# Kernel tuning notes

Measured on AMD Instinct MI355X. Metric: run time of the kernel, lower is better.

The kernel has to match this reference:

```python
import math
import jax, jax.numpy as jnp
import numpy as np

D, H, L, DFF, V = 512, 8, 6, 2048, 32000
B, S = 2, 2048
PAD = 1


def _layernorm(x, g, b, eps=1e-5):
    m = x.mean(-1, keepdims=True)
    v = ((x - m) ** 2).mean(-1, keepdims=True)
    return (x - m) / jnp.sqrt(v + eps) * g + b


def _mha(qx, kx, w, b, mask, h=H):
    # w: [4, D, D] (q,k,v,out), b: [4, D]; mask broadcastable to [B,1,Sq,Sk]
    bs, sq, d = qx.shape
    dk = d // h
    def proj(x, i):
        return (x @ w[i] + b[i]).reshape(bs, -1, h, dk).transpose(0, 2, 1, 3)
    q, k, v = proj(qx, 0), proj(kx, 1), proj(kx, 2)
    scores = jnp.einsum('bhqd,bhkd->bhqk', q, k) / math.sqrt(dk)
    scores = jnp.where(mask, scores, -jnp.inf)
    attn = jax.nn.softmax(scores, axis=-1)
    out = jnp.einsum('bhqk,bhkd->bhqd', attn, v).transpose(0, 2, 1, 3).reshape(bs, sq, d)
    return out @ w[3] + b[3]


def _ff(x, w1, b1, w2, b2):
    return jax.nn.relu(x @ w1 + b1) @ w2 + b2


def _sinusoidal_pe(max_len, d):
    pos = np.arange(max_len)[:, None].astype(np.float64)
    div = np.exp(np.arange(0, d, 2) * (-math.log(10000.0) / d))
    pe = np.zeros((max_len, d), np.float32)
    pe[:, 0::2] = np.sin(pos * div)
    pe[:, 1::2] = np.cos(pos * div)
    return jnp.asarray(pe[None])  # [1, max_len, d]


def setup_inputs() -> dict:
    key = jax.random.key(0)
    ks = iter(jax.random.split(key, 32))
    def w(shape):
        return jax.random.normal(next(ks), shape, jnp.float32) * 0.02
    inp = {
        'src': jax.random.randint(next(ks), (B, S), 2, V),
        'tgt': jax.random.randint(next(ks), (B, S), 2, V),
        'src_emb': w((V, D)),
        'tgt_emb': w((V, D)),
        'pe': _sinusoidal_pe(S, D),
        'enc_attn_w': w((L, 4, D, D)), 'enc_attn_b': jnp.zeros((L, 4, D)),
        'enc_ff_w1': w((L, D, DFF)), 'enc_ff_b1': jnp.zeros((L, DFF)),
        'enc_ff_w2': w((L, DFF, D)), 'enc_ff_b2': jnp.zeros((L, D)),
        'enc_ln_g': jnp.ones((L, 2, D)), 'enc_ln_b': jnp.zeros((L, 2, D)),
        'dec_self_w': w((L, 4, D, D)), 'dec_self_b': jnp.zeros((L, 4, D)),
        'dec_src_w': w((L, 4, D, D)), 'dec_src_b': jnp.zeros((L, 4, D)),
        'dec_ff_w1': w((L, D, DFF)), 'dec_ff_b1': jnp.zeros((L, DFF)),
        'dec_ff_w2': w((L, DFF, D)), 'dec_ff_b2': jnp.zeros((L, D)),
        'dec_ln_g': jnp.ones((L, 3, D)), 'dec_ln_b': jnp.zeros((L, 3, D)),
        'ln_g': jnp.ones((D,)), 'ln_b': jnp.zeros((D,)),
        'fc_w': w((D, V)), 'fc_b': jnp.zeros((V,)),
    }
    return inp


def reference(src, tgt, src_emb, tgt_emb, pe,
              enc_attn_w, enc_attn_b, enc_ff_w1, enc_ff_b1, enc_ff_w2, enc_ff_b2,
              enc_ln_g, enc_ln_b,
              dec_self_w, dec_self_b, dec_src_w, dec_src_b,
              dec_ff_w1, dec_ff_b1, dec_ff_w2, dec_ff_b2, dec_ln_g, dec_ln_b,
              ln_g, ln_b, fc_w, fc_b):
    s_len, t_len = src.shape[1], tgt.shape[1]
    src_mask = (src != PAD)[:, None, None, :]                      # [B,1,1,Ss]
    tril = jnp.tril(jnp.ones((t_len, t_len), bool))
    tgt_mask = (tgt != PAD)[:, None, None, :] & tril[None, None]   # [B,1,St,St]

    x = src_emb[src] + pe[:, :s_len]
    for l in range(L):
        x2 = _layernorm(x, enc_ln_g[l, 0], enc_ln_b[l, 0])
        x = x + _mha(x2, x2, enc_attn_w[l], enc_attn_b[l], src_mask)
        x2 = _layernorm(x, enc_ln_g[l, 1], enc_ln_b[l, 1])
        x = x + _ff(x2, enc_ff_w1[l], enc_ff_b1[l], enc_ff_w2[l], enc_ff_b2[l])
    memory = x

    y = tgt_emb[tgt] + pe[:, :t_len]
    for l in range(L):
        y2 = _layernorm(y, dec_ln_g[l, 0], dec_ln_b[l, 0])
        y = y + _mha(y2, y2, dec_self_w[l], dec_self_b[l], tgt_mask)
        y2 = _layernorm(y, dec_ln_g[l, 1], dec_ln_b[l, 1])
        y = y + _mha(y2, memory, dec_src_w[l], dec_src_b[l], src_mask)
        y2 = _layernorm(y, dec_ln_g[l, 2], dec_ln_b[l, 2])
        y = y + _ff(y2, dec_ff_w1[l], dec_ff_b1[l], dec_ff_w2[l], dec_ff_b2[l])

    return _layernorm(y, ln_g, ln_b) @ fc_w + fc_b  # [B, St, V]
```

## Files before the change

### kernel.cpp

```cpp
#include <hip/hip_runtime.h>
#include <math.h>

#define D_MODEL 512
#define NHEAD   8
#define NLAYER  6
#define DFF_    2048
#define VOCAB   32000
#define BATCH   2
#define SEQ     2048
#define NTOK    (BATCH*SEQ)
#define PAD_ID  1

typedef __attribute__((ext_vector_type(8))) short s16x8;
typedef __attribute__((ext_vector_type(4))) float f32x4;
typedef unsigned short u16;
typedef unsigned int   u32;
typedef unsigned long long u64;

__device__ __forceinline__ u16 f2bf(float x) {
  u32 u = __builtin_bit_cast(u32, x);
  u += 0x7FFFu + ((u >> 16) & 1u);
  return (u16)(u >> 16);
}

__device__ __forceinline__ float exp2i(float x) {
  float r; asm("v_exp_f32 %0, %1" : "=v"(r) : "v"(x)); return r;
}

__device__ __forceinline__ void gload16(const void* g, void* l) {
  __builtin_amdgcn_global_load_lds(
      (const __attribute__((address_space(1))) u32*)g,
      (__attribute__((address_space(3))) u32*)l, 16, 0, 0);
}

#define CEXP 0.1803368802f

__global__ __launch_bounds__(256) void embed2_kernel(
    const int* __restrict__ src, const int* __restrict__ tgt,
    const float* __restrict__ se, const float* __restrict__ te,
    const float* __restrict__ pe, float* __restrict__ xe, float* __restrict__ yd)
{
  const int z = blockIdx.y;
  const int* tok = z ? tgt : src;
  const float* emb = z ? te : se;
  float* out = z ? yd : xe;
  const int total = NTOK * D_MODEL;
  for (int i = blockIdx.x * 256 + threadIdx.x; i < total; i += gridDim.x * 256) {
    int t = i >> 9;
    int d = i & 511;
    int s = t & (SEQ - 1);
    out[i] = emb[(size_t)tok[t] * D_MODEL + d] + pe[(size_t)s * D_MODEL + d];
  }
}

__global__ __launch_bounds__(64) void padmask2_kernel(
    const int* __restrict__ src, const int* __restrict__ tgt,
    u64* __restrict__ pmS, u64* __restrict__ pmT)
{
  const int z = blockIdx.z;
  const int* tok = z ? tgt : src;
  u64* pm = z ? pmT : pmS;
  int b = blockIdx.y, t = blockIdx.x;
  int lane = threadIdx.x;
  u64 m = __ballot(tok[(size_t)b * SEQ + t * 64 + lane] != PAD_ID);
  if (lane == 0) pm[b * (SEQ / 64) + t] = m;
}

__global__ __launch_bounds__(256) void ln_kernel(
    const float* __restrict__ x, const float* __restrict__ g,
    const float* __restrict__ bb, u16* __restrict__ y)
{
  __shared__ float red[8];
  const size_t row = blockIdx.x;
  const float* xr = x + row * D_MODEL;
  u16* yr = y + row * D_MODEL;
  const int t = threadIdx.x;
  float a0 = xr[t], a1 = xr[t + 256];
  float s = a0 + a1;
  #pragma unroll
  for (int o = 32; o > 0; o >>= 1) s += __shfl_down(s, o, 64);
  int wv = t >> 6, ln = t & 63;
  if (ln == 0) red[wv] = s;
  __syncthreads();
  if (t == 0) red[4] = red[0] + red[1] + red[2] + red[3];
  __syncthreads();
  float mean = red[4] * (1.0f / D_MODEL);
  float d0 = a0 - mean, d1 = a1 - mean;
  float vs = d0 * d0 + d1 * d1;
  #pragma unroll
  for (int o = 32; o > 0; o >>= 1) vs += __shfl_down(vs, o, 64);
  if (ln == 0) red[wv] = vs;
  __syncthreads();
  if (t == 0) red[5] = red[0] + red[1] + red[2] + red[3];
  __syncthreads();
  float inv = rsqrtf(red[5] * (1.0f / D_MODEL) + 1e-5f);
  yr[t]       = f2bf(d0 * inv * g[t]       + bb[t]);
  yr[t + 256] = f2bf(d1 * inv * g[t + 256] + bb[t + 256]);
}

__global__ __launch_bounds__(256) void tconv2_kernel(
    const float* __restrict__ s0, const float* __restrict__ s1,
    u16* __restrict__ d0, u16* __restrict__ d1, int zsplit, int K, int N)
{
  __shared__ float tile[64][65];
  const int z = blockIdx.z;
  const float* src = (z < zsplit) ? s0 + (size_t)z * K * N : s1 + (size_t)(z - zsplit) * K * N;
  u16* dst = (z < zsplit) ? d0 + (size_t)z * K * N : d1 + (size_t)(z - zsplit) * K * N;
  const int n0 = blockIdx.x * 64, k0 = blockIdx.y * 64;
  const int t = threadIdx.x;
  const int cr = t >> 4, cc = (t & 15) * 4;
  #pragma unroll
  for (int it = 0; it < 4; ++it) {
    int kr = cr + it * 16;
    float4 v = *(const float4*)&src[(size_t)(k0 + kr) * N + n0 + cc];
    tile[kr][cc] = v.x; tile[kr][cc + 1] = v.y; tile[kr][cc + 2] = v.z; tile[kr][cc + 3] = v.w;
  }
  __syncthreads();
  #pragma unroll
  for (int it = 0; it < 4; ++it) {
    int nr = cr + it * 16;
    u32 lo = (u32)f2bf(tile[cc + 0][nr]) | ((u32)f2bf(tile[cc + 1][nr]) << 16);
    u32 hi = (u32)f2bf(tile[cc + 2][nr]) | ((u32)f2bf(tile[cc + 3][nr]) << 16);
    uint2 pk; pk.x = lo; pk.y = hi;
    *(uint2*)&dst[(size_t)(n0 + nr) * K + k0 + cc] = pk;
  }
}

__global__ __launch_bounds__(256) void tconv3_kernel(
    const float* __restrict__ s0, const float* __restrict__ s1,
    const float* __restrict__ s2, u16* __restrict__ dst0)
{
  __shared__ float tile[64][65];
  const int z = blockIdx.z;
  const float* src = (z < 24) ? s0 + (size_t)z * 262144
                   : (z < 48) ? s1 + (size_t)(z - 24) * 262144
                              : s2 + (size_t)(z - 48) * 262144;
  u16* dst = dst0 + (size_t)z * 262144;
  const int n0 = blockIdx.x * 64, k0 = blockIdx.y * 64;
  const int t = threadIdx.x;
  const int cr = t >> 4, cc = (t & 15) * 4;
  #pragma unroll
  for (int it = 0; it < 4; ++it) {
    int kr = cr + it * 16;
    float4 v = *(const float4*)&src[(size_t)(k0 + kr) * 512 + n0 + cc];
    tile[kr][cc] = v.x; tile[kr][cc + 1] = v.y; tile[kr][cc + 2] = v.z; tile[kr][cc + 3] = v.w;
  }
  __syncthreads();
  #pragma unroll
  for (int it = 0; it < 4; ++it) {
    int nr = cr + it * 16;
    u32 lo = (u32)f2bf(tile[cc + 0][nr]) | ((u32)f2bf(tile[cc + 1][nr]) << 16);
    u32 hi = (u32)f2bf(tile[cc + 2][nr]) | ((u32)f2bf(tile[cc + 3][nr]) << 16);
    uint2 pk; pk.x = lo; pk.y = hi;
    *(uint2*)&dst[(size_t)(n0 + nr) * 512 + k0 + cc] = pk;
  }
}

template<int MODE, int BM, int BN, int MAP>
__global__ __launch_bounds__(256, 2) void mm_kernel(
    const u16* __restrict__ A, const u16* __restrict__ Wt,
    const float* __restrict__ bias, const float* __restrict__ res,
    void* __restrict__ Cout, u16* __restrict__ vtOut,
    int M, int N, int K,
    long long wStride, long long bStride, long long cStride)
{
  constexpr int MI = BM / 32;
  constexpr int NI = BN / 32;
  constexpr bool DB = (BM == 64 && BN == 64);
  __shared__ u16 sh[(DB ? 2 : 1) * (BM + BN) * 64];
  const int z = blockIdx.z;
  size_t wOff, bOff;
  if (MAP == 1) {
    wOff = (size_t)(z >> 1) * 4 * 262144 + (size_t)(1 + (z & 1)) * 262144;
    bOff = (size_t)(z >> 1) * 4 * 512 + (size_t)(1 + (z & 1)) * 512;
  } else {
    wOff = (size_t)z * wStride;
    bOff = (size_t)z * bStride;
  }
  Wt += wOff;
  bias += bOff;
  const int bm = blockIdx.y * BM, bn = blockIdx.x * BN;
  const int tid = threadIdx.x, lane = tid & 63, w = tid >> 6;
  const int wm = w >> 1, wn = w & 1;
  const int l15 = lane & 15, l4 = lane >> 4;
  const int wrow0 = wm * (BM / 2), wcol0 = wn * (BN / 2);
  const u16* aBase = A  + (size_t)bm * K;
  const u16* bBase = Wt + (size_t)bn * K;
  f32x4 acc[MI][NI] = {};

  auto mfma_step = [&](const u16* Asb, const u16* Bsb) {
    #pragma unroll
    for (int ks = 0; ks < 2; ++ks) {
      s16x8 af[MI], bf[NI];
      #pragma unroll
      for (int mi = 0; mi < MI; ++mi) {
        int rr = wrow0 + mi * 16 + l15;
        af[mi] = *(const s16x8*)&Asb[(rr << 6) + (((ks * 4 + l4) ^ (rr & 7)) << 3)];
      }
      #pragma unroll
      for (int ni = 0; ni < NI; ++ni) {
        int rr = wcol0 + ni * 16 + l15;
        bf[ni] = *(const s16x8*)&Bsb[(rr << 6) + (((ks * 4 + l4) ^ (rr & 7)) << 3)];
      }
      #pragma unroll
      for (int mi = 0; mi < MI; ++mi)
        #pragma unroll
        for (int ni = 0; ni < NI; ++ni)
          acc[mi][ni] = __builtin_amdgcn_mfma_f32_16x16x32_bf16(af[mi], bf[ni], acc[mi][ni], 0, 0, 0);
    }
  };

  if constexpr (DB) {
    u16* As0 = sh;
    u16* As1 = sh + 64 * 64;
    u16* Bs0 = sh + 2 * 64 * 64;
    u16* Bs1 = sh + 3 * 64 * 64;
    auto stage = [&](int k0, u16* Ad, u16* Bd) {
      #pragma unroll
      for (int i = 0; i < 2; ++i) {
        int lin = i * 256 + tid;
        int r = lin >> 3, sp = lin & 7;
        gload16(aBase + (size_t)r * K + k0 + ((sp ^ (r & 7)) * 8), &Ad[(i * 256 + w * 64) * 8]);
      }
      #pragma unroll
      for (int i = 0; i < 2; ++i) {
        int lin = i * 256 + tid;
        int r = lin >> 3, sp = lin & 7;
        gload16(bBase + (size_t)r * K + k0 + ((sp ^ (r & 7)) * 8), &Bd[(i * 256 + w * 64) * 8]);
      }
    };
    stage(0, As0, Bs0);
    __syncthreads();
    const int nt = K >> 6;
    for (int t = 0; t < nt; ++t) {
      const bool even = !(t & 1);
      u16* Ac = even ? As0 : As1;
      u16* Bc = even ? Bs0 : Bs1;
      if (t + 1 < nt) stage((t + 1) << 6, even ? As1 : As0, even ? Bs1 : Bs0);
      mfma_step(Ac, Bc);
      __syncthreads();
    }
  } else {
    u16* As = sh;
    u16* Bs = sh + BM * 64;
    for (int k0 = 0; k0 < K; k0 += 64) {
      #pragma unroll
      for (int i = 0; i < BM / 32; ++i) {
        int lin = i * 256 + tid;
        int r = lin >> 3, sp = lin & 7;
        gload16(aBase + (size_t)r * K + k0 + ((sp ^ (r & 7)) * 8), &As[(i * 256 + w * 64) * 8]);
      }
      #pragma unroll
      for (int i = 0; i < BN / 32; ++i) {
        int lin = i * 256 + tid;
        int r = lin >> 3, sp = lin & 7;
        gload16(bBase + (size_t)r * K + k0 + ((sp ^ (r & 7)) * 8), &Bs[(i * 256 + w * 64) * 8]);
      }
      __syncthreads();
      mfma_step(As, Bs);
      __syncthreads();
    }
  }

  const bool vpath = (MODE == 4 && z == 2) || (MODE == 5 && (z & 1) == 1);
  if (vpath) {
    u16* TT = sh;
    #pragma unroll
    for (int mi = 0; mi < MI; ++mi)
      #pragma unroll
      for (int ni = 0; ni < NI; ++ni)
        #pragma unroll
        for (int r = 0; r < 4; ++r) {
          int rowl = wrow0 + mi * 16 + l4 * 4 + r;
          int coll = wcol0 + ni * 16 + l15;
          TT[coll * 72 + rowl] = f2bf(acc[mi][ni][r] + bias[bn + coll]);
        }
    __syncthreads();
    const int b = bm >> 11, s0loc = bm & 2047, h = bn >> 6;
    const int layer = (MODE == 5) ? (z >> 1) : 0;
    u16* vbase = vtOut + (size_t)layer * ((size_t)NTOK * D_MODEL)
               + ((size_t)(b * NHEAD + h) * 64) * SEQ;
    int d = tid >> 2, sc = (tid & 3) * 16;
    s16x8 v0 = *(const s16x8*)&TT[d * 72 + sc];
    s16x8 v1 = *(const s16x8*)&TT[d * 72 + sc + 8];
    *(s16x8*)(vbase + (size_t)d * SEQ + s0loc + sc) = v0;
    *(s16x8*)(vbase + (size_t)d * SEQ + s0loc + sc + 8) = v1;
    return;
  }

  const int zi = (MAP == 1) ? (z >> 1) : z;
  #pragma unroll
  for (int ni = 0; ni < NI; ++ni) {
    int col = bn + wcol0 + ni * 16 + l15;
    float bb = bias[col];
    #pragma unroll
    for (int mi = 0; mi < MI; ++mi) {
      #pragma unroll
      for (int r = 0; r < 4; ++r) {
        int row = bm + wrow0 + mi * 16 + l4 * 4 + r;
        size_t off = (size_t)zi * cStride + (size_t)row * N + col;
        float v = acc[mi][ni][r] + bb;
        if (MODE == 1 || MODE == 6) v += res[(size_t)row * N + col];
        if (MODE == 3) v = fmaxf(v, 0.0f);
        if (MODE <= 1 || MODE == 6) ((float*)Cout)[off] = v;
        else                        ((u16*)Cout)[off] = f2bf(v);
        if (MODE == 6) vtOut[(size_t)row * N + col] = f2bf(v);
      }
    }
  }
}

template<int CAUSAL, int QPROJ>
__global__ __launch_bounds__(256, 2) void fattn_kernel(
    const u16* __restrict__ Qg, const u16* __restrict__ Kg,
    const u16* __restrict__ Vt, const u16* __restrict__ Wq,
    const float* __restrict__ qbias, const u64* __restrict__ padm,
    u16* __restrict__ Og)
{
  __shared__ u16 Ks[2][128 * 64];
  __shared__ u16 Vs[2][64 * 128];
  __shared__ u16 Ps[4][16 * 128];
  const int qtile = CAUSAL ? (int)(gridDim.x - 1 - blockIdx.x) : (int)blockIdx.x;
  const int qt = qtile * 64;
  const int h = blockIdx.y, b = blockIdx.z;
  const int tid = threadIdx.x, lane = tid & 63, w = tid >> 6;
  const int l15 = lane & 15, l4 = lane >> 4;
  const int hoff = h * 64;
  const u16* Kbase = Kg + (size_t)(b * SEQ) * D_MODEL + hoff;
  const u16* Vbase = Vt + (size_t)(b * NHEAD + h) * 64 * SEQ;
  const u64* pmb = padm + b * (SEQ / 64);

  s16x8 aq[2];
  if constexpr (QPROJ) {
    const u16* xBase = Qg + (size_t)(b * SEQ + qt) * D_MODEL;
    const u16* wBase = Wq + (size_t)hoff * D_MODEL;
    u16* Xs = Ks[0];
    u16* Wsh = Ks[0] + 64 * 64;
    f32x4 qa[4] = {};
    for (int k0 = 0; k0 < 512; k0 += 64) {
      #pragma unroll
      for (int i = 0; i < 2; ++i) {
        int lin = i * 256 + tid;
        int r = lin >> 3, sp = lin & 7;
        gload16(xBase + (size_t)r * D_MODEL + k0 + ((sp ^ (r & 7)) * 8), &Xs[(i * 256 + w * 64) * 8]);
      }
      #pragma unroll
      for (int i = 0; i < 2; ++i) {
        int lin = i * 256 + tid;
        int r = lin >> 3, sp = lin & 7;
        gload16(wBase + (size_t)r * D_MODEL + k0 + ((sp ^ (r & 7)) * 8), &Wsh[(i * 256 + w * 64) * 8]);
      }
      __syncthreads();
      #pragma unroll
      for (int ks = 0; ks < 2; ++ks) {
        int rr = w * 16 + l15;
        s16x8 xa = *(const s16x8*)&Xs[(rr << 6) + (((ks * 4 + l4) ^ (rr & 7)) << 3)];
        #pragma unroll
        for (int ni = 0; ni < 4; ++ni) {
          int rw = ni * 16 + l15;
          s16x8 wb = *(const s16x8*)&Wsh[(rw << 6) + (((ks * 4 + l4) ^ (rw & 7)) << 3)];
          qa[ni] = __builtin_amdgcn_mfma_f32_16x16x32_bf16(xa, wb, qa[ni], 0, 0, 0);
        }
      }
      __syncthreads();
    }
    u16* Qsh = (u16*)Ps;
    #pragma unroll
    for (int ni = 0; ni < 4; ++ni) {
      int col = ni * 16 + l15;
      float bb = qbias[hoff + col];
      #pragma unroll
      for (int r = 0; r < 4; ++r) {
        int row = w * 16 + l4 * 4 + r;
        Qsh[(row << 6) + ((((col >> 3)) ^ (row & 7)) << 3) + (col & 7)] = f2bf(qa[ni][r] + bb);
      }
    }
    __syncthreads();
    {
      int rr = w * 16 + l15;
      aq[0] = *(const s16x8*)&Qsh[(rr << 6) + (((0 + l4) ^ (rr & 7)) << 3)];
      aq[1] = *(const s16x8*)&Qsh[(rr << 6) + (((4 + l4) ^ (rr & 7)) << 3)];
    }
  } else {
    const u16* qp = Qg + (size_t)(b * SEQ + qt + w * 16 + l15) * D_MODEL + hoff + l4 * 8;
    aq[0] = *(const s16x8*)qp;
    aq[1] = *(const s16x8*)(qp + 32);
  }

  f32x4 oacc[4] = {};
  float mrow[4] = {-1e30f, -1e30f, -1e30f, -1e30f};
  float lrow[4] = {0.f, 0.f, 0.f, 0.f};
  const int nt = CAUSAL ? (qt >> 7) + 1 : SEQ / 128;

  #define STAGE(KV0, BUF)                                                              \
    {                                                                                  \
      _Pragma("unroll")                                                                \
      for (int it = 0; it < 4; ++it) {                                                 \
        int lin = it * 256 + tid;                                                      \
        int rr = lin >> 3, sp = lin & 7;                                               \
        gload16(Kbase + (size_t)((KV0) + rr) * D_MODEL + ((sp ^ (rr & 7)) * 8),        \
                &Ks[BUF][(it * 256 + w * 64) * 8]);                                    \
      }                                                                                \
      _Pragma("unroll")                                                                \
      for (int it = 0; it < 4; ++it) {                                                 \
        int lin = it * 256 + tid;                                                      \
        int rr = lin >> 4, ko = lin & 15;                                              \
        gload16(Vbase + (size_t)rr * SEQ + (KV0) + ((ko ^ (rr & 15)) * 8),             \
                &Vs[BUF][(it * 256 + w * 64) * 8]);                                    \
      }                                                                                \
    }

  if constexpr (QPROJ) __syncthreads();
  STAGE(0, 0);
  __syncthreads();

  for (int kt = 0; kt < nt; ++kt) {
    const int kv0 = kt * 128;
    const int cur = kt & 1;
    if (kt + 1 < nt) STAGE(kv0 + 128, cur ^ 1);

    f32x4 sac[8] = {};
    #pragma unroll
    for (int ks = 0; ks < 2; ++ks)
      #pragma unroll
      for (int jn = 0; jn < 8; ++jn) {
        int rr = jn * 16 + l15;
        s16x8 bk = *(const s16x8*)&Ks[cur][(rr << 6) + (((ks * 4 + l4) ^ (rr & 7)) << 3)];
        sac[jn] = __builtin_amdgcn_mfma_f32_16x16x32_bf16(aq[ks], bk, sac[jn], 0, 0, 0);
      }

    const u64 m0 = pmb[(kv0 >> 6)];
    const u64 m1 = pmb[(kv0 >> 6) + 1];
    const bool lastC = CAUSAL && (kt == nt - 1);
    if (((m0 & m1) != ~0ull) || lastC) {
      #pragma unroll
      for (int jn = 0; jn < 8; ++jn) {
        int kvg = kv0 + jn * 16 + l15;
        u64 mm = (jn < 4) ? m0 : m1;
        bool okp = (mm >> ((jn & 3) * 16 + l15)) & 1;
        #pragma unroll
        for (int r = 0; r < 4; ++r) {
          int qg = qt + w * 16 + l4 * 4 + r;
          bool ok = okp && (!CAUSAL || kvg <= qg);
          if (!ok) sac[jn][r] = -1e30f;
        }
      }
    }

    float mx[4];
    #pragma unroll
    for (int r = 0; r < 4; ++r) {
      float m = fmaxf(fmaxf(fmaxf(sac[0][r], sac[1][r]), fmaxf(sac[2][r], sac[3][r])),
                      fmaxf(fmaxf(sac[4][r], sac[5][r]), fmaxf(sac[6][r], sac[7][r])));
      #pragma unroll
      for (int o = 1; o < 16; o <<= 1) m = fmaxf(m, __shfl_xor(m, o, 16));
      mx[r] = m;
    }
    float growth = fmaxf(fmaxf(mx[0] - mrow[0], mx[1] - mrow[1]),
                         fmaxf(mx[2] - mrow[2], mx[3] - mrow[3]));
    if (__any(growth > 64.0f)) {
      #pragma unroll
      for (int r = 0; r < 4; ++r) {
        float mn = fmaxf(mrow[r], mx[r]);
        float sc = exp2i((mrow[r] - mn) * CEXP);
        mrow[r] = mn;
        lrow[r] *= sc;
        #pragma unroll
        for (int jn = 0; jn < 4; ++jn) oacc[jn][r] *= sc;
      }
    }

    #pragma unroll
    for (int r = 0; r < 4; ++r) {
      const int prow = l4 * 4 + r;
      float rs = 0.f;
      #pragma unroll
      for (int jn = 0; jn < 8; ++jn) {
        float pv = exp2i((sac[jn][r] - mrow[r]) * CEXP);
        rs += pv;
        int g = ((jn * 2 + (l15 >> 3)) ^ prow) & 15;
        Ps[w][prow * 128 + g * 8 + (l15 & 7)] = f2bf(pv);
      }
      #pragma unroll
      for (int o = 1; o < 16; o <<= 1) rs += __shfl_xor(rs, o, 16);
      lrow[r] += rs;
    }

    #pragma unroll
    for (int kslot = 0; kslot < 4; ++kslot) {
      s16x8 pa = *(const s16x8*)&Ps[w][l15 * 128 + ((((kslot * 4 + l4) ^ l15) & 15) << 3)];
      #pragma unroll
      for (int jn = 0; jn < 4; ++jn) {
        int rr = jn * 16 + l15;
        s16x8 bv = *(const s16x8*)&Vs[cur][(rr << 7) + (((kslot * 4 + l4) ^ (rr & 15)) << 3)];
        oacc[jn] = __builtin_amdgcn_mfma_f32_16x16x32_bf16(pa, bv, oacc[jn], 0, 0, 0);
      }
    }
    __syncthreads();
  }
  #undef STAGE

  float inv[4];
  #pragma unroll
  for (int r = 0; r < 4; ++r) inv[r] = 1.0f / lrow[r];
  #pragma unroll
  for (int jn = 0; jn < 4; ++jn)
    #pragma unroll
    for (int r = 0; r < 4; ++r)
      Og[(size_t)(b * SEQ + qt + w * 16 + l4 * 4 + r) * D_MODEL + hoff + jn * 16 + l15] =
          f2bf(oacc[jn][r] * inv[r]);
}

extern "C" void kernel_launch(void* const* d_in, const int* in_sizes, int n_in,
                              void* d_out, int out_size, void* d_ws, size_t ws_size,
                              hipStream_t stream)
{
  const int*   src        = (const int*)  d_in[0];
  const int*   tgt        = (const int*)  d_in[1];
  const float* src_emb    = (const float*)d_in[2];
  const float* tgt_emb    = (const float*)d_in[3];
  const float* pe         = (const float*)d_in[4];
  const float* enc_attn_w = (const float*)d_in[5];
  const float* enc_attn_b = (const float*)d_in[6];
  const float* enc_ff_w1  = (const float*)d_in[7];
  const float* enc_ff_b1  = (const float*)d_in[8];
  const float* enc_ff_w2  = (const float*)d_in[9];
  const float* enc_ff_b2  = (const float*)d_in[10];
  const float* enc_ln_g   = (const float*)d_in[11];
  const float* enc_ln_bb  = (const float*)d_in[12];
  const float* dec_self_w = (const float*)d_in[13];
  const float* dec_self_b = (const float*)d_in[14];
  const float* dec_src_w  = (const float*)d_in[15];
  const float* dec_src_b  = (const float*)d_in[16];
  const float* dec_ff_w1  = (const float*)d_in[17];
  const float* dec_ff_b1  = (const float*)d_in[18];
  const float* dec_ff_w2  = (const float*)d_in[19];
  const float* dec_ff_b2  = (const float*)d_in[20];
  const float* dec_ln_g   = (const float*)d_in[21];
  const float* dec_ln_bb  = (const float*)d_in[22];
  const float* fin_ln_g   = (const float*)d_in[23];
  const float* fin_ln_b   = (const float*)d_in[24];
  const float* fc_w       = (const float*)d_in[25];
  const float* fc_b       = (const float*)d_in[26];
  float* out = (float*)d_out;

  const size_t DD = (size_t)D_MODEL * D_MODEL;
  const size_t FD = (size_t)D_MODEL * DFF_;
  const size_t TD = (size_t)NTOK * D_MODEL;

  char* ob = (char*)d_out;
  size_t off = 0;
  auto alloco = [&](size_t bytes) { void* p = ob + off; off += (bytes + 255) & ~(size_t)255; return p; };
  u16* wt_enc_attn = (u16*)alloco(24 * DD * 2);
  u16* wt_dec_self = (u16*)alloco(24 * DD * 2);
  u16* wt_dec_src  = (u16*)alloco(24 * DD * 2);
  u16* wt_enc_ff1  = (u16*)alloco(6 * FD * 2);
  u16* wt_enc_ff2  = (u16*)alloco(6 * FD * 2);
  u16* wt_dec_ff1  = (u16*)alloco(6 * FD * 2);
  u16* wt_dec_ff2  = (u16*)alloco(6 * FD * 2);
  u16* qb   = (u16*)alloco(2 * TD * 2);
  u16* kb   = qb + TD;
  u16* vtb  = (u16*)alloco(TD * 2);
  u16* aob  = (u16*)alloco(TD * 2);
  u16* hbb  = (u16*)alloco((size_t)NTOK * DFF_ * 2);
  u16* memb = (u16*)alloco(TD * 2);
  u16* ckb  = (u16*)alloco(6 * TD * 2);
  u16* cvtb = (u16*)alloco(6 * TD * 2);

  char* wsb = (char*)d_ws;
  u16*   fcwt = (u16*)wsb;
  size_t wo = ((size_t)VOCAB * D_MODEL * 2 + 255) & ~(size_t)255;
  float* xe  = (float*)(wsb + wo); wo += TD * 4;
  float* yd  = (float*)(wsb + wo); wo += TD * 4;
  u16*   x2b = (u16*)(wsb + wo);   wo += TD * 2;
  u64*   pmS = (u64*)(wsb + wo);   wo += 1024;
  u64*   pmT = (u64*)(wsb + wo);

  dim3 blk(256);
  dim3 gN512(8, 64, 1), gQKV(8, 64, 3), gCKV(8, 64, 12);
  dim3 gFF1(16, 32, 1), gFC(125, 32, 1);
  dim3 gAttn(SEQ / 64, NHEAD, BATCH);
  const long long llDD = (long long)DD, llTD = (long long)TD;

  padmask2_kernel<<<dim3(SEQ / 64, BATCH, 2), dim3(64), 0, stream>>>(src, tgt, pmS, pmT);
  tconv3_kernel<<<dim3(8, 8, 72), blk, 0, stream>>>(enc_attn_w, dec_self_w, dec_src_w, wt_enc_attn);
  tconv2_kernel<<<dim3(32, 8, 12), blk, 0, stream>>>(enc_ff_w1, dec_ff_w1, wt_enc_ff1, wt_dec_ff1, 6, 512, 2048);
  tconv2_kernel<<<dim3(8, 32, 12), blk, 0, stream>>>(enc_ff_w2, dec_ff_w2, wt_enc_ff2, wt_dec_ff2, 6, 2048, 512);
  tconv2_kernel<<<dim3(500, 8, 1), blk, 0, stream>>>(fc_w, fc_w, fcwt, fcwt, 1, 512, VOCAB);
  embed2_kernel<<<dim3(2048, 2), blk, 0, stream>>>(src, tgt, src_emb, tgt_emb, pe, xe, yd);

  for (int l = 0; l < NLAYER; ++l) {
    ln_kernel<<<dim3(NTOK), blk, 0, stream>>>(xe, enc_ln_g + (size_t)(l * 2 + 0) * D_MODEL,
                                              enc_ln_bb + (size_t)(l * 2 + 0) * D_MODEL, x2b);
    mm_kernel<4, 64, 64, 0><<<gQKV, blk, 0, stream>>>(x2b, wt_enc_attn + (size_t)l * 4 * DD,
        enc_attn_b + (size_t)l * 4 * D_MODEL, nullptr, qb, vtb, NTOK, 512, 512, llDD, D_MODEL, llTD);
    fattn_kernel<0, 0><<<gAttn, blk, 0, stream>>>(qb, kb, vtb, nullptr, nullptr, pmS, aob);
    mm_kernel<1, 64, 64, 0><<<gN512, blk, 0, stream>>>(aob, wt_enc_attn + (size_t)(l * 4 + 3) * DD,
        enc_attn_b + (size_t)(l * 4 + 3) * D_MODEL, xe, xe, nullptr, NTOK, 512, 512, 0, 0, 0);
    ln_kernel<<<dim3(NTOK), blk, 0, stream>>>(xe, enc_ln_g + (size_t)(l * 2 + 1) * D_MODEL,
                                              enc_ln_bb + (size_t)(l * 2 + 1) * D_MODEL, x2b);
    mm_kernel<3, 128, 128, 0><<<gFF1, blk, 0, stream>>>(x2b, wt_enc_ff1 + (size_t)l * FD,
        enc_ff_b1 + (size_t)l * DFF_, nullptr, hbb, nullptr, NTOK, DFF_, 512, 0, 0, 0);
    if (l == NLAYER - 1)
      mm_kernel<6, 64, 64, 0><<<gN512, blk, 0, stream>>>(hbb, wt_enc_ff2 + (size_t)l * FD,
          enc_ff_b2 + (size_t)l * D_MODEL, xe, xe, memb, NTOK, 512, DFF_, 0, 0, 0);
    else
      mm_kernel<1, 64, 64, 0><<<gN512, blk, 0, stream>>>(hbb, wt_enc_ff2 + (size_t)l * FD,
          enc_ff_b2 + (size_t)l * D_MODEL, xe, xe, nullptr, NTOK, 512, DFF_, 0, 0, 0);
  }

  mm_kernel<5, 64, 64, 1><<<gCKV, blk, 0, stream>>>(memb, wt_dec_src, dec_src_b, nullptr,
      ckb, cvtb, NTOK, 512, 512, 0, 0, llTD);

  for (int l = 0; l < NLAYER; ++l) {
    const u16* Ws = wt_dec_self + (size_t)l * 4 * DD;
    const u16* Wc = wt_dec_src + (size_t)l * 4 * DD;
    const float* bs  = dec_self_b + (size_t)l * 4 * D_MODEL;
    const float* bcb = dec_src_b + (size_t)l * 4 * D_MODEL;
    ln_kernel<<<dim3(NTOK), blk, 0, stream>>>(yd, dec_ln_g + (size_t)(l * 3 + 0) * D_MODEL,
                                              dec_ln_bb + (size_t)(l * 3 + 0) * D_MODEL, x2b);
    mm_kernel<4, 64, 64, 0><<<gQKV, blk, 0, stream>>>(x2b, Ws, bs, nullptr, qb, vtb,
                                                      NTOK, 512, 512, llDD, D_MODEL, llTD);
    fattn_kernel<1, 0><<<gAttn, blk, 0, stream>>>(qb, kb, vtb, nullptr, nullptr, pmT, aob);
    mm_kernel<1, 64, 64, 0><<<gN512, blk, 0, stream>>>(aob, Ws + 3 * DD, bs + 3 * D_MODEL, yd, yd,
                                                       nullptr, NTOK, 512, 512, 0, 0, 0);
    ln_kernel<<<dim3(NTOK), blk, 0, stream>>>(yd, dec_ln_g + (size_t)(l * 3 + 1) * D_MODEL,
                                              dec_ln_bb + (size_t)(l * 3 + 1) * D_MODEL, x2b);
    fattn_kernel<0, 1><<<gAttn, blk, 0, stream>>>(x2b, ckb + (size_t)l * TD, cvtb + (size_t)l * TD,
                                                  Wc, bcb, pmS, aob);
    mm_kernel<1, 64, 64, 0><<<gN512, blk, 0, stream>>>(aob, Wc + 3 * DD, bcb + 3 * D_MODEL, yd, yd,
                                                       nullptr, NTOK, 512, 512, 0, 0, 0);
    ln_kernel<<<dim3(NTOK), blk, 0, stream>>>(yd, dec_ln_g + (size_t)(l * 3 + 2) * D_MODEL,
                                              dec_ln_bb + (size_t)(l * 3 + 2) * D_MODEL, x2b);
    mm_kernel<3, 128, 128, 0><<<gFF1, blk, 0, stream>>>(x2b, wt_dec_ff1 + (size_t)l * FD,
        dec_ff_b1 + (size_t)l * DFF_, nullptr, hbb, nullptr, NTOK, DFF_, 512, 0, 0, 0);
    mm_kernel<1, 64, 64, 0><<<gN512, blk, 0, stream>>>(hbb, wt_dec_ff2 + (size_t)l * FD,
        dec_ff_b2 + (size_t)l * D_MODEL, yd, yd, nullptr, NTOK, 512, DFF_, 0, 0, 0);
  }

  ln_kernel<<<dim3(NTOK), blk, 0, stream>>>(yd, fin_ln_g, fin_ln_b, x2b);
  mm_kernel<0, 128, 256, 0><<<gFC, blk, 0, stream>>>(x2b, fcwt, fc_b, nullptr, out, nullptr,
                                                     NTOK, VOCAB, 512, 0, 0, 0);

  (void)in_sizes; (void)n_in; (void)out_size; (void)ws_size;
}
```

Measured before the change: 2.503 ms.

## Transpose attention MFMA operands and make LayerNorm one row per wavefront

The flash-attention kernel swaps the MFMA operand order so each lane holds scores for a single query row. That collapses the per-row max and sum to scalar state with two cross-lane shuffles, and lets P and output stores use packed vector writes. LayerNorm now processes four rows per block, one wavefront each, with vectorized float4 loads and single-pass sum and sum-of-squares reductions, removing shared memory and barriers. The single-pass variance formula is slightly less numerically robust than the two-pass version.

```diff
diff --git a/kernel.cpp b/kernel.cpp
--- a/kernel.cpp
+++ b/kernel.cpp
@@ -70,32 +70,31 @@
     const float* __restrict__ x, const float* __restrict__ g,
     const float* __restrict__ bb, u16* __restrict__ y)
 {
-  __shared__ float red[8];
-  const size_t row = blockIdx.x;
-  const float* xr = x + row * D_MODEL;
-  u16* yr = y + row * D_MODEL;
-  const int t = threadIdx.x;
-  float a0 = xr[t], a1 = xr[t + 256];
-  float s = a0 + a1;
+  const int lane = threadIdx.x & 63;
+  const size_t row = (size_t)blockIdx.x * 4 + (threadIdx.x >> 6);
+  const float* xr = x + row * D_MODEL + lane * 8;
+  float4 v0 = *(const float4*)xr;
+  float4 v1 = *(const float4*)(xr + 4);
+  float sum = (v0.x + v0.y) + (v0.z + v0.w) + (v1.x + v1.y) + (v1.z + v1.w);
+  float ss = v0.x * v0.x + v0.y * v0.y + v0.z * v0.z + v0.w * v0.w
+           + v1.x * v1.x + v1.y * v1.y + v1.z * v1.z + v1.w * v1.w;
   #pragma unroll
-  for (int o = 32; o > 0; o >>= 1) s += __shfl_down(s, o, 64);
-  int wv = t >> 6, ln = t & 63;
-  if (ln == 0) red[wv] = s;
-  __syncthreads();
-  if (t == 0) red[4] = red[0] + red[1] + red[2] + red[3];
-  __syncthreads();
-  float mean = red[4] * (1.0f / D_MODEL);
-  float d0 = a0 - mean, d1 = a1 - mean;
-  float vs = d0 * d0 + d1 * d1;
-  #pragma unroll
-  for (int o = 32; o > 0; o >>= 1) vs += __shfl_down(vs, o, 64);
-  if (ln == 0) red[wv] = vs;
-  __syncthreads();
-  if (t == 0) red[5] = red[0] + red[1] + red[2] + red[3];
-  __syncthreads();
-  float inv = rsqrtf(red[5] * (1.0f / D_MODEL) + 1e-5f);
-  yr[t]       = f2bf(d0 * inv * g[t]       + bb[t]);
-  yr[t + 256] = f2bf(d1 * inv * g[t + 256] + bb[t + 256]);
+  for (int o = 1; o < 64; o <<= 1) {
+    sum += __shfl_xor(sum, o, 64);
+    ss  += __shfl_xor(ss, o, 64);
+  }
+  float mean = sum * (1.0f / D_MODEL);
+  float inv = rsqrtf(ss * (1.0f / D_MODEL) - mean * mean + 1e-5f);
+  float4 g0 = *(const float4*)&g[lane * 8];
+  float4 g1 = *(const float4*)&g[lane * 8 + 4];
+  float4 c0 = *(const float4*)&bb[lane * 8];
+  float4 c1 = *(const float4*)&bb[lane * 8 + 4];
+  uint4 o;
+  o.x = (u32)f2bf((v0.x - mean) * inv * g0.x + c0.x) | ((u32)f2bf((v0.y - mean) * inv * g0.y + c0.y) << 16);
+  o.y = (u32)f2bf((v0.z - mean) * inv * g0.z + c0.z) | ((u32)f2bf((v0.w - mean) * inv * g0.w + c0.w) << 16);
+  o.z = (u32)f2bf((v1.x - mean) * inv * g1.x + c1.x) | ((u32)f2bf((v1.y - mean) * inv * g1.y + c1.y) << 16);
+  o.w = (u32)f2bf((v1.z - mean) * inv * g1.z + c1.z) | ((u32)f2bf((v1.w - mean) * inv * g1.w + c1.w) << 16);
+  *(uint4*)&y[row * D_MODEL + lane * 8] = o;
 }
 
 __global__ __launch_bounds__(256) void tconv2_kernel(
@@ -329,6 +328,7 @@
   const u16* Kbase = Kg + (size_t)(b * SEQ) * D_MODEL + hoff;
   const u16* Vbase = Vt + (size_t)(b * NHEAD + h) * 64 * SEQ;
   const u64* pmb = padm + b * (SEQ / 64);
+  const int qg = qt + w * 16 + l15;
 
   s16x8 aq[2];
   if constexpr (QPROJ) {
@@ -382,14 +382,13 @@
       aq[1] = *(const s16x8*)&Qsh[(rr << 6) + (((4 + l4) ^ (rr & 7)) << 3)];
     }
   } else {
-    const u16* qp = Qg + (size_t)(b * SEQ + qt + w * 16 + l15) * D_MODEL + hoff + l4 * 8;
+    const u16* qp = Qg + (size_t)(b * SEQ + qg) * D_MODEL + hoff + l4 * 8;
     aq[0] = *(const s16x8*)qp;
     aq[1] = *(const s16x8*)(qp + 32);
   }
 
   f32x4 oacc[4] = {};
-  float mrow[4] = {-1e30f, -1e30f, -1e30f, -1e30f};
-  float lrow[4] = {0.f, 0.f, 0.f, 0.f};
+  float mrow = -1e30f, lrow = 0.f;
   const int nt = CAUSAL ? (qt >> 7) + 1 : SEQ / 128;
 
   #define STAGE(KV0, BUF)                                                              \
@@ -425,8 +424,8 @@
       #pragma unroll
       for (int jn = 0; jn < 8; ++jn) {
         int rr = jn * 16 + l15;
-        s16x8 bk = *(const s16x8*)&Ks[cur][(rr << 6) + (((ks * 4 + l4) ^ (rr & 7)) << 3)];
-        sac[jn] = __builtin_amdgcn_mfma_f32_16x16x32_bf16(aq[ks], bk, sac[jn], 0, 0, 0);
+        s16x8 ak = *(const s16x8*)&Ks[cur][(rr << 6) + (((ks * 4 + l4) ^ (rr & 7)) << 3)];
+        sac[jn] = __builtin_amdgcn_mfma_f32_16x16x32_bf16(ak, aq[ks], sac[jn], 0, 0, 0);
       }
 
     const u64 m0 = pmb[(kv0 >> 6)];
@@ -435,80 +434,78 @@
     if (((m0 & m1) != ~0ull) || lastC) {
       #pragma unroll
       for (int jn = 0; jn < 8; ++jn) {
-        int kvg = kv0 + jn * 16 + l15;
         u64 mm = (jn < 4) ? m0 : m1;
-        bool okp = (mm >> ((jn & 3) * 16 + l15)) & 1;
         #pragma unroll
         for (int r = 0; r < 4; ++r) {
-          int qg = qt + w * 16 + l4 * 4 + r;
-          bool ok = okp && (!CAUSAL || kvg <= qg);
+          int kl = (jn & 3) * 16 + l4 * 4 + r;
+          int kvg = kv0 + jn * 16 + l4 * 4 + r;
+          bool ok = ((mm >> kl) & 1) && (!CAUSAL || kvg <= qg);
           if (!ok) sac[jn][r] = -1e30f;
         }
       }
     }
 
-    float mx[4];
-    #pragma unroll
-    for (int r = 0; r < 4; ++r) {
-      float m = fmaxf(fmaxf(fmaxf(sac[0][r], sac[1][r]), fmaxf(sac[2][r], sac[3][r])),
-                      fmaxf(fmaxf(sac[4][r], sac[5][r]), fmaxf(sac[6][r], sac[7][r])));
-      #pragma unroll
-      for (int o = 1; o < 16; o <<= 1) m = fmaxf(m, __shfl_xor(m, o, 16));
-      mx[r] = m;
-    }
-    float growth = fmaxf(fmaxf(mx[0] - mrow[0], mx[1] - mrow[1]),
-                         fmaxf(mx[2] - mrow[2], mx[3] - mrow[3]));
-    if (__any(growth > 64.0f)) {
-      #pragma unroll
-      for (int r = 0; r < 4; ++r) {
-        float mn = fmaxf(mrow[r], mx[r]);
-        float sc = exp2i((mrow[r] - mn) * CEXP);
-        mrow[r] = mn;
-        lrow[r] *= sc;
+    float m = sac[0][0];
+    #pragma unroll
+    for (int jn = 0; jn < 8; ++jn)
+      #pragma unroll
+      for (int r = 0; r < 4; ++r) m = fmaxf(m, sac[jn][r]);
+    m = fmaxf(m, __shfl_xor(m, 16, 64));
+    m = fmaxf(m, __shfl_xor(m, 32, 64));
+
+    if (__any(m - mrow > 64.0f)) {
+      float mn = fmaxf(mrow, m);
+      float sc = exp2i((mrow - mn) * CEXP);
+      mrow = mn;
+      lrow *= sc;
+      #pragma unroll
+      for (int jn = 0; jn < 4; ++jn)
         #pragma unroll
-        for (int jn = 0; jn < 4; ++jn) oacc[jn][r] *= sc;
-      }
-    }
-
-    #pragma unroll
-    for (int r = 0; r < 4; ++r) {
-      const int prow = l4 * 4 + r;
-      float rs = 0.f;
-      #pragma unroll
-      for (int jn = 0; jn < 8; ++jn) {
-        float pv = exp2i((sac[jn][r] - mrow[r]) * CEXP);
-        rs += pv;
-        int g = ((jn * 2 + (l15 >> 3)) ^ prow) & 15;
-        Ps[w][prow * 128 + g * 8 + (l15 & 7)] = f2bf(pv);
-      }
-      #pragma unroll
-      for (int o = 1; o < 16; o <<= 1) rs += __shfl_xor(rs, o, 16);
-      lrow[r] += rs;
-    }
-
-    #pragma unroll
-    for (int kslot = 0; kslot < 4; ++kslot) {
-      s16x8 pa = *(const s16x8*)&Ps[w][l15 * 128 + ((((kslot * 4 + l4) ^ l15) & 15) << 3)];
+        for (int r = 0; r < 4; ++r) oacc[jn][r] *= sc;
+    }
+
+    float rs = 0.f;
+    #pragma unroll
+    for (int jn = 0; jn < 8; ++jn) {
+      float p0 = exp2i((sac[jn][0] - mrow) * CEXP);
+      float p1 = exp2i((sac[jn][1] - mrow) * CEXP);
+      float p2 = exp2i((sac[jn][2] - mrow) * CEXP);
+      float p3 = exp2i((sac[jn][3] - mrow) * CEXP);
+      rs += (p0 + p1) + (p2 + p3);
+      uint2 pk;
+      pk.x = (u32)f2bf(p0) | ((u32)f2bf(p1) << 16);
+      pk.y = (u32)f2bf(p2) | ((u32)f2bf(p3) << 16);
+      int pu = (jn * 4 + l4) ^ ((l15 & 7) << 2);
+      *(uint2*)&Ps[w][l15 * 128 + pu * 4] = pk;
+    }
+    rs += __shfl_xor(rs, 16, 64);
+    rs += __shfl_xor(rs, 32, 64);
+    lrow += rs;
+
+    #pragma unroll
+    for (int ks2 = 0; ks2 < 4; ++ks2) {
+      int pu = (ks2 * 8 + l4 * 2) ^ ((l15 & 7) << 2);
+      s16x8 pb = *(const s16x8*)&Ps[w][l15 * 128 + pu * 4];
       #pragma unroll
       for (int jn = 0; jn < 4; ++jn) {
         int rr = jn * 16 + l15;
-        s16x8 bv = *(const s16x8*)&Vs[cur][(rr << 7) + (((kslot * 4 + l4) ^ (rr & 15)) << 3)];
-        oacc[jn] = __builtin_amdgcn_mfma_f32_16x16x32_bf16(pa, bv, oacc[jn], 0, 0, 0);
+        s16x8 av = *(const s16x8*)&Vs[cur][(rr << 7) + (((ks2 * 4 + l4) ^ (rr & 15)) << 3)];
+        oacc[jn] = __builtin_amdgcn_mfma_f32_16x16x32_bf16(av, pb, oacc[jn], 0, 0, 0);
       }
     }
     __syncthreads();
   }
   #undef STAGE
 
-  float inv[4];
+  const float inv = 1.0f / lrow;
+  u16* orow = Og + (size_t)(b * SEQ + qg) * D_MODEL + hoff;
   #pragma unroll
-  for (int r = 0; r < 4; ++r) inv[r] = 1.0f / lrow[r];
-  #pragma unroll
-  for (int jn = 0; jn < 4; ++jn)
-    #pragma unroll
-    for (int r = 0; r < 4; ++r)
-      Og[(size_t)(b * SEQ + qt + w * 16 + l4 * 4 + r) * D_MODEL + hoff + jn * 16 + l15] =
-          f2bf(oacc[jn][r] * inv[r]);
+  for (int jn = 0; jn < 4; ++jn) {
+    uint2 pk;
+    pk.x = (u32)f2bf(oacc[jn][0] * inv) | ((u32)f2bf(oacc[jn][1] * inv) << 16);
+    pk.y = (u32)f2bf(oacc[jn][2] * inv) | ((u32)f2bf(oacc[jn][3] * inv) << 16);
+    *(uint2*)(orow + jn * 16 + l4 * 4) = pk;
+  }
 }
 
 extern "C" void kernel_launch(void* const* d_in, const int* in_sizes, int n_in,
@@ -580,6 +577,7 @@
   dim3 gN512(8, 64, 1), gQKV(8, 64, 3), gCKV(8, 64, 12);
   dim3 gFF1(16, 32, 1), gFC(125, 32, 1);
   dim3 gAttn(SEQ / 64, NHEAD, BATCH);
+  dim3 gLN(NTOK / 4);
   const long long llDD = (long long)DD, llTD = (long long)TD;
 
   padmask2_kernel<<<dim3(SEQ / 64, BATCH, 2), dim3(64), 0, stream>>>(src, tgt, pmS, pmT);
@@ -590,15 +588,15 @@
   embed2_kernel<<<dim3(2048, 2), blk, 0, stream>>>(src, tgt, src_emb, tgt_emb, pe, xe, yd);
 
   for (int l = 0; l < NLAYER; ++l) {
-    ln_kernel<<<dim3(NTOK), blk, 0, stream>>>(xe, enc_ln_g + (size_t)(l * 2 + 0) * D_MODEL,
-                                              enc_ln_bb + (size_t)(l * 2 + 0) * D_MODEL, x2b);
+    ln_kernel<<<gLN, blk, 0, stream>>>(xe, enc_ln_g + (size_t)(l * 2 + 0) * D_MODEL,
+                                       enc_ln_bb + (size_t)(l * 2 + 0) * D_MODEL, x2b);
     mm_kernel<4, 64, 64, 0><<<gQKV, blk, 0, stream>>>(x2b, wt_enc_attn + (size_t)l * 4 * DD,
         enc_attn_b + (size_t)l * 4 * D_MODEL, nullptr, qb, vtb, NTOK, 512, 512, llDD, D_MODEL, llTD);
     fattn_kernel<0, 0><<<gAttn, blk, 0, stream>>>(qb, kb, vtb, nullptr, nullptr, pmS, aob);
     mm_kernel<1, 64, 64, 0><<<gN512, blk, 0, stream>>>(aob, wt_enc_attn + (size_t)(l * 4 + 3) * DD,
         enc_attn_b + (size_t)(l * 4 + 3) * D_MODEL, xe, xe, nullptr, NTOK, 512, 512, 0, 0, 0);
-    ln_kernel<<<dim3(NTOK), blk, 0, stream>>>(xe, enc_ln_g + (size_t)(l * 2 + 1) * D_MODEL,
-                                              enc_ln_bb + (size_t)(l * 2 + 1) * D_MODEL, x2b);
+    ln_kernel<<<gLN, blk, 0, stream>>>(xe, enc_ln_g + (size_t)(l * 2 + 1) * D_MODEL,
+                                       enc_ln_bb + (size_t)(l * 2 + 1) * D_MODEL, x2b);
     mm_kernel<3, 128, 128, 0><<<gFF1, blk, 0, stream>>>(x2b, wt_enc_ff1 + (size_t)l * FD,
         enc_ff_b1 + (size_t)l * DFF_, nullptr, hbb, nullptr, NTOK, DFF_, 512, 0, 0, 0);
     if (l == NLAYER - 1)
@@ -617,28 +615,28 @@
     const u16* Wc = wt_dec_src + (size_t)l * 4 * DD;
     const float* bs  = dec_self_b + (size_t)l * 4 * D_MODEL;
     const float* bcb = dec_src_b + (size_t)l * 4 * D_MODEL;
-    ln_kernel<<<dim3(NTOK), blk, 0, stream>>>(yd, dec_ln_g + (size_t)(l * 3 + 0) * D_MODEL,
-                                              dec_ln_bb + (size_t)(l * 3 + 0) * D_MODEL, x2b);
+    ln_kernel<<<gLN, blk, 0, stream>>>(yd, dec_ln_g + (size_t)(l * 3 + 0) * D_MODEL,
+                                       dec_ln_bb + (size_t)(l * 3 + 0) * D_MODEL, x2b);
     mm_kernel<4, 64, 64, 0><<<gQKV, blk, 0, stream>>>(x2b, Ws, bs, nullptr, qb, vtb,
                                                       NTOK, 512, 512, llDD, D_MODEL, llTD);
     fattn_kernel<1, 0><<<gAttn, blk, 0, stream>>>(qb, kb, vtb, nullptr, nullptr, pmT, aob);
     mm_kernel<1, 64, 64, 0><<<gN512, blk, 0, stream>>>(aob, Ws + 3 * DD, bs + 3 * D_MODEL, yd, yd,
                                                        nullptr, NTOK, 512, 512, 0, 0, 0);
-    ln_kernel<<<dim3(NTOK), blk, 0, stream>>>(yd, dec_ln_g + (size_t)(l * 3 + 1) * D_MODEL,
-                                              dec_ln_bb + (size_t)(l * 3 + 1) * D_MODEL, x2b);
+    ln_kernel<<<gLN, blk, 0, stream>>>(yd, dec_ln_g + (size_t)(l * 3 + 1) * D_MODEL,
+                                       dec_ln_bb + (size_t)(l * 3 + 1) * D_MODEL, x2b);
     fattn_kernel<0, 1><<<gAttn, blk, 0, stream>>>(x2b, ckb + (size_t)l * TD, cvtb + (size_t)l * TD,
                                                   Wc, bcb, pmS, aob);
     mm_kernel<1, 64, 64, 0><<<gN512, blk, 0, stream>>>(aob, Wc + 3 * DD, bcb + 3 * D_MODEL, yd, yd,
                                                        nullptr, NTOK, 512, 512, 0, 0, 0);
-    ln_kernel<<<dim3(NTOK), blk, 0, stream>>>(yd, dec_ln_g + (size_t)(l * 3 + 2) * D_MODEL,
-                                              dec_ln_bb + (size_t)(l * 3 + 2) * D_MODEL, x2b);
+    ln_kernel<<<gLN, blk, 0, stream>>>(yd, dec_ln_g + (size_t)(l * 3 + 2) * D_MODEL,
+                                       dec_ln_bb + (size_t)(l * 3 + 2) * D_MODEL, x2b);
     mm_kernel<3, 128, 128, 0><<<gFF1, blk, 0, stream>>>(x2b, wt_dec_ff1 + (size_t)l * FD,
         dec_ff_b1 + (size_t)l * DFF_, nullptr, hbb, nullptr, NTOK, DFF_, 512, 0, 0, 0);
     mm_kernel<1, 64, 64, 0><<<gN512, blk, 0, stream>>>(hbb, wt_dec_ff2 + (size_t)l * FD,
         dec_ff_b2 + (size_t)l * D_MODEL, yd, yd, nullptr, NTOK, 512, DFF_, 0, 0, 0);
   }
 
-  ln_kernel<<<dim3(NTOK), blk, 0, stream>>>(yd, fin_ln_g, fin_ln_b, x2b);
+  ln_kernel<<<gLN, blk, 0, stream>>>(yd, fin_ln_g, fin_ln_b, x2b);
   mm_kernel<0, 128, 256, 0><<<gFC, blk, 0, stream>>>(x2b, fcwt, fc_b, nullptr, out, nullptr,
                                                      NTOK, VOCAB, 512, 0, 0, 0);
 
```

New measurement: 2.285 ms. 1.1x faster.
